# Optimization experiments

Hardware: AMD Instinct MI355X
Metric: run time of the kernel (lower is better)

## Reference

```python
import jax, jax.numpy as jnp
import numpy as np

NUM_SEGMENTS = 4480  # BATCH_SIZE * MAX_ATOMS = 64 * 70
ATOM_DIM = 64
BOND_DIM = 16
N_EDGES = 65536


def setup_inputs() -> dict:
    key = jax.random.key(0)
    k1, k2, k3, k4 = jax.random.split(key, 4)
    atom_feat = jax.random.normal(k1, (NUM_SEGMENTS, ATOM_DIM), dtype=jnp.float32)
    bond_feat = jax.random.normal(k2, (N_EDGES, BOND_DIM), dtype=jnp.float32)
    pair_idx = jax.random.randint(k3, (N_EDGES, 2), 0, NUM_SEGMENTS, dtype=jnp.int64)
    # glorot-uniform style kernel, zero bias (as in add_weight initializers)
    limit = float(np.sqrt(6.0 / (BOND_DIM + ATOM_DIM ** 2)))
    kernel = jax.random.uniform(k4, (BOND_DIM, ATOM_DIM ** 2), dtype=jnp.float32,
                                minval=-limit, maxval=limit)
    bias = jnp.zeros((ATOM_DIM ** 2,), dtype=jnp.float32)
    return {"atom_feat": atom_feat, "bond_feat": bond_feat,
            "pair_idx": pair_idx, "kernel": kernel, "bias": bias}


def reference(atom_feat, bond_feat, pair_idx, kernel, bias):
    atom_dim = atom_feat.shape[-1]
    # dense projection of bond features -> per-edge transform matrices
    bond_transformed = bond_feat @ kernel + bias               # [E, D*D]
    bond_transformed = bond_transformed.reshape(-1, atom_dim, atom_dim)  # [E, D, D]
    # gather neighbor (source) atom features per edge
    neighbor_feat = jnp.take(atom_feat, pair_idx[:, 1].astype(jnp.int32), axis=0)  # [E, D]
    # per-edge matrix-vector product
    messages = jnp.einsum('eij,ej->ei', bond_transformed, neighbor_feat)  # [E, D]
    # scatter-add into destination atoms
    return jax.ops.segment_sum(messages, pair_idx[:, 0].astype(jnp.int32),
                               num_segments=NUM_SEGMENTS)  # [NUM_SEGMENTS, D]
```

## Files before the change

kernel.cpp:

```cpp
#include <hip/hip_runtime.h>

#define NSEG   4480
#define ADIM   64
#define BDIM   16
#define NEDGE  65536
#define DPB    16
#define NBLK   (NSEG / DPB)
#define TPB    512
#define CAP    64
#define GSP    1096

#define CNT_OFF  (4u << 20)

typedef __bf16 bf16x8 __attribute__((ext_vector_type(8)));
typedef float  f32x4  __attribute__((ext_vector_type(4)));

__device__ __forceinline__ unsigned short f2bf(float f) {
    union { float f; unsigned int i; } c; c.f = f;
    unsigned int x = c.i;
    x += 0x7fffu + ((x >> 16) & 1u);
    return (unsigned short)(x >> 16);
}

union U8 { unsigned short u[8]; bf16x8 v; };

__device__ __forceinline__ bf16x8 pack_bf8(float4 a, float4 b) {
    U8 r;
    r.u[0] = f2bf(a.x); r.u[1] = f2bf(a.y); r.u[2] = f2bf(a.z); r.u[3] = f2bf(a.w);
    r.u[4] = f2bf(b.x); r.u[5] = f2bf(b.y); r.u[6] = f2bf(b.z); r.u[7] = f2bf(b.w);
    return r.v;
}

__device__ __forceinline__ void load_bond16(const float* __restrict__ bond,
                                            int e, float* bb) {
    const float4* bp = (const float4*)(bond + (size_t)e * BDIM);
    const float4 c0 = bp[0], c1 = bp[1], c2 = bp[2], c3 = bp[3];
    bb[0]=c0.x;  bb[1]=c0.y;  bb[2]=c0.z;  bb[3]=c0.w;
    bb[4]=c1.x;  bb[5]=c1.y;  bb[6]=c1.z;  bb[7]=c1.w;
    bb[8]=c2.x;  bb[9]=c2.y;  bb[10]=c2.z; bb[11]=c2.w;
    bb[12]=c3.x; bb[13]=c3.y; bb[14]=c3.z; bb[15]=c3.w;
}

__global__ __launch_bounds__(256) void scatter_kernel(
    const int* __restrict__ pair, int* __restrict__ cnt, int2* __restrict__ eb)
{
    const int e  = blockIdx.x * 256 + threadIdx.x;
    const int2 p = ((const int2*)pair)[e];
    const int idx = atomicAdd(&cnt[p.x], 1);
    if (idx < CAP) eb[(size_t)p.x * CAP + idx] = make_int2(e, p.y);
}

__global__ __launch_bounds__(TPB) void fused_kernel(
    const float* __restrict__ atom,
    const float* __restrict__ bond,
    const int*   __restrict__ cnt,
    const int2*  __restrict__ eb,
    const float* __restrict__ kern,
    const float* __restrict__ bias,
    float*       __restrict__ out)
{
    __shared__ unsigned short Gs[DPB * GSP];
    __shared__ f32x4 pb[4][64];

    const int t    = threadIdx.x;
    const int lane = t & 63;
    const int w    = t >> 6;
    const int dlo  = blockIdx.x * DPB;

    {
        const int da = dlo + 2 * w;
        const int db = da + 1;
        int na = cnt[da]; na = na < CAP ? na : CAP;
        int nb = cnt[db]; nb = nb < CAP ? nb : CAP;
        const int2 mya = eb[(size_t)da * CAP + lane];
        const int2 myb = eb[(size_t)db * CAP + lane];

        float ga[17], gb[17];
#pragma unroll
        for (int r = 0; r < 17; ++r) { ga[r] = 0.f; gb[r] = 0.f; }

        const int nmax = na > nb ? na : nb;
        for (int k = 0; k < nmax; k += 2) {
            const bool va0 = k < na, va1 = k + 1 < na;
            const bool vb0 = k < nb, vb1 = k + 1 < nb;
            int ea0 = __builtin_amdgcn_readlane(mya.x, k);
            int sa0 = __builtin_amdgcn_readlane(mya.y, k);
            int ea1 = __builtin_amdgcn_readlane(mya.x, k + 1);
            int sa1 = __builtin_amdgcn_readlane(mya.y, k + 1);
            int eb0 = __builtin_amdgcn_readlane(myb.x, k);
            int sb0 = __builtin_amdgcn_readlane(myb.y, k);
            int eb1 = __builtin_amdgcn_readlane(myb.x, k + 1);
            int sb1 = __builtin_amdgcn_readlane(myb.y, k + 1);
            ea0 = va0 ? ea0 : 0;  sa0 = va0 ? sa0 : 0;
            ea1 = va1 ? ea1 : 0;  sa1 = va1 ? sa1 : 0;
            eb0 = vb0 ? eb0 : 0;  sb0 = vb0 ? sb0 : 0;
            eb1 = vb1 ? eb1 : 0;  sb1 = vb1 ? sb1 : 0;

            const float aa0 = atom[(size_t)sa0 * ADIM + lane] * (va0 ? 1.f : 0.f);
            const float aa1 = atom[(size_t)sa1 * ADIM + lane] * (va1 ? 1.f : 0.f);
            const float ab0 = atom[(size_t)sb0 * ADIM + lane] * (vb0 ? 1.f : 0.f);
            const float ab1 = atom[(size_t)sb1 * ADIM + lane] * (vb1 ? 1.f : 0.f);
            float ba0[16], ba1[16], bb0[16], bb1[16];
            load_bond16(bond, ea0, ba0);
            load_bond16(bond, ea1, ba1);
            load_bond16(bond, eb0, bb0);
            load_bond16(bond, eb1, bb1);

#pragma unroll
            for (int r = 0; r < 16; ++r) {
                ga[r] = fmaf(aa0, ba0[r], ga[r]);
                ga[r] = fmaf(aa1, ba1[r], ga[r]);
                gb[r] = fmaf(ab0, bb0[r], gb[r]);
                gb[r] = fmaf(ab1, bb1[r], gb[r]);
            }
            ga[16] += aa0 + aa1;
            gb[16] += ab0 + ab1;
        }

#pragma unroll
        for (int r = 0; r < 17; ++r) {
            Gs[(2 * w) * GSP + r * 64 + lane]     = f2bf(ga[r]);
            Gs[(2 * w + 1) * GSP + r * 64 + lane] = f2bf(gb[r]);
        }
    }
    __syncthreads();

    {
        const int kh   = w >> 2;
        const int ct   = w & 3;
        const int m    = lane & 15;
        const int quad = lane >> 4;
        const int c    = ct * 16 + m;
        const unsigned short* Ga = Gs + (size_t)m * GSP;
        const int rlo = kh ? 9 : 0;
        const int rhi = kh ? 17 : 9;

        f32x4 acc = {0.f, 0.f, 0.f, 0.f};

        const float* ks0 = ((rlo < 16) ? (kern + (size_t)rlo * 4096) : bias)
                           + (size_t)c * 64 + quad * 8;
        float4 x0 = *(const float4*)(ks0);
        float4 x1 = *(const float4*)(ks0 + 4);
        float4 y0 = *(const float4*)(ks0 + 32);
        float4 y1 = *(const float4*)(ks0 + 36);

        for (int r = rlo; r < rhi; ++r) {
            float4 nx0 = {}, nx1 = {}, ny0 = {}, ny1 = {};
            if (r + 1 < rhi) {
                const float* ns = ((r + 1 < 16) ? (kern + (size_t)(r + 1) * 4096)
                                                : bias)
                                  + (size_t)c * 64 + quad * 8;
                nx0 = *(const float4*)(ns);
                nx1 = *(const float4*)(ns + 4);
                ny0 = *(const float4*)(ns + 32);
                ny1 = *(const float4*)(ns + 36);
            }
            const bf16x8 a0 = *(const bf16x8*)(Ga + r * 64 + quad * 8);
            const bf16x8 a1 = *(const bf16x8*)(Ga + r * 64 + 32 + quad * 8);
            acc = __builtin_amdgcn_mfma_f32_16x16x32_bf16(a0, pack_bf8(x0, x1), acc, 0, 0, 0);
            acc = __builtin_amdgcn_mfma_f32_16x16x32_bf16(a1, pack_bf8(y0, y1), acc, 0, 0, 0);
            x0 = nx0; x1 = nx1; y0 = ny0; y1 = ny1;
        }

        if (kh) pb[ct][lane] = acc;
        __syncthreads();
        if (!kh) {
            const f32x4 p = pb[ct][lane];
            acc[0] += p[0]; acc[1] += p[1]; acc[2] += p[2]; acc[3] += p[3];
#pragma unroll
            for (int rr = 0; rr < 4; ++rr)
                out[(size_t)(dlo + quad * 4 + rr) * ADIM + c] = acc[rr];
        }
    }
}

extern "C" void kernel_launch(void* const* d_in, const int* in_sizes, int n_in,
                              void* d_out, int out_size, void* d_ws, size_t ws_size,
                              hipStream_t stream) {
    const float* atom = (const float*)d_in[0];
    const float* bond = (const float*)d_in[1];
    const int*   pair = (const int*)  d_in[2];
    const float* kern = (const float*)d_in[3];
    const float* bias = (const float*)d_in[4];
    float* out = (float*)d_out;

    int2* eb  = (int2*)d_ws;
    int*  cnt = (int*)((char*)d_ws + CNT_OFF);

    hipMemsetAsync(cnt, 0, NSEG * sizeof(int), stream);
    scatter_kernel<<<NEDGE / 256, 256, 0, stream>>>(pair, cnt, eb);
    fused_kernel<<<NBLK, TPB, 0, stream>>>(atom, bond, cnt, eb, kern, bias, out);
}
```

Baseline: 112.3 us.

## Cooperatively load 16 edges per wave via LDS staging and readlane broadcast of bond features

The per-destination gather phase now has each wave load 16 edges at once. Each group of 4 lanes fetches one edge's atom row and bond vector, stages the atom rows in a per-wave LDS tile, and then broadcasts the bond values with readlane. Before, every lane redundantly loaded full 16-float bond vectors per edge. The change also processes the two destinations sequentially instead of interleaved and adds an occupancy hint to launch bounds. The cost is extra LDS traffic and many readlane instructions, and the wave-local LDS reuse relies only on a waitcnt rather than a barrier.

```diff
diff --git a/kernel.cpp b/kernel.cpp
--- a/kernel.cpp
+++ b/kernel.cpp
@@ -9,6 +9,7 @@
 #define TPB    512
 #define CAP    64
 #define GSP    1096
+#define ALP    68
 
 #define CNT_OFF  (4u << 20)
 
@@ -31,14 +32,9 @@
     return r.v;
 }
 
-__device__ __forceinline__ void load_bond16(const float* __restrict__ bond,
-                                            int e, float* bb) {
-    const float4* bp = (const float4*)(bond + (size_t)e * BDIM);
-    const float4 c0 = bp[0], c1 = bp[1], c2 = bp[2], c3 = bp[3];
-    bb[0]=c0.x;  bb[1]=c0.y;  bb[2]=c0.z;  bb[3]=c0.w;
-    bb[4]=c1.x;  bb[5]=c1.y;  bb[6]=c1.z;  bb[7]=c1.w;
-    bb[8]=c2.x;  bb[9]=c2.y;  bb[10]=c2.z; bb[11]=c2.w;
-    bb[12]=c3.x; bb[13]=c3.y; bb[14]=c3.z; bb[15]=c3.w;
+__device__ __forceinline__ float rl(float v, int l) {
+    return __builtin_bit_cast(float,
+        __builtin_amdgcn_readlane(__builtin_bit_cast(int, v), l));
 }
 
 __global__ __launch_bounds__(256) void scatter_kernel(
@@ -50,7 +46,7 @@
     if (idx < CAP) eb[(size_t)p.x * CAP + idx] = make_int2(e, p.y);
 }
 
-__global__ __launch_bounds__(TPB) void fused_kernel(
+__global__ __launch_bounds__(TPB, 4) void fused_kernel(
     const float* __restrict__ atom,
     const float* __restrict__ bond,
     const int*   __restrict__ cnt,
@@ -60,68 +56,70 @@
     float*       __restrict__ out)
 {
     __shared__ unsigned short Gs[DPB * GSP];
+    __shared__ float Al[8][16 * ALP];
     __shared__ f32x4 pb[4][64];
 
     const int t    = threadIdx.x;
     const int lane = t & 63;
     const int w    = t >> 6;
     const int dlo  = blockIdx.x * DPB;
-
-    {
-        const int da = dlo + 2 * w;
-        const int db = da + 1;
-        int na = cnt[da]; na = na < CAP ? na : CAP;
-        int nb = cnt[db]; nb = nb < CAP ? nb : CAP;
-        const int2 mya = eb[(size_t)da * CAP + lane];
-        const int2 myb = eb[(size_t)db * CAP + lane];
-
-        float ga[17], gb[17];
-#pragma unroll
-        for (int r = 0; r < 17; ++r) { ga[r] = 0.f; gb[r] = 0.f; }
-
-        const int nmax = na > nb ? na : nb;
-        for (int k = 0; k < nmax; k += 2) {
-            const bool va0 = k < na, va1 = k + 1 < na;
-            const bool vb0 = k < nb, vb1 = k + 1 < nb;
-            int ea0 = __builtin_amdgcn_readlane(mya.x, k);
-            int sa0 = __builtin_amdgcn_readlane(mya.y, k);
-            int ea1 = __builtin_amdgcn_readlane(mya.x, k + 1);
-            int sa1 = __builtin_amdgcn_readlane(mya.y, k + 1);
-            int eb0 = __builtin_amdgcn_readlane(myb.x, k);
-            int sb0 = __builtin_amdgcn_readlane(myb.y, k);
-            int eb1 = __builtin_amdgcn_readlane(myb.x, k + 1);
-            int sb1 = __builtin_amdgcn_readlane(myb.y, k + 1);
-            ea0 = va0 ? ea0 : 0;  sa0 = va0 ? sa0 : 0;
-            ea1 = va1 ? ea1 : 0;  sa1 = va1 ? sa1 : 0;
-            eb0 = vb0 ? eb0 : 0;  sb0 = vb0 ? sb0 : 0;
-            eb1 = vb1 ? eb1 : 0;  sb1 = vb1 ? sb1 : 0;
-
-            const float aa0 = atom[(size_t)sa0 * ADIM + lane] * (va0 ? 1.f : 0.f);
-            const float aa1 = atom[(size_t)sa1 * ADIM + lane] * (va1 ? 1.f : 0.f);
-            const float ab0 = atom[(size_t)sb0 * ADIM + lane] * (vb0 ? 1.f : 0.f);
-            const float ab1 = atom[(size_t)sb1 * ADIM + lane] * (vb1 ? 1.f : 0.f);
-            float ba0[16], ba1[16], bb0[16], bb1[16];
-            load_bond16(bond, ea0, ba0);
-            load_bond16(bond, ea1, ba1);
-            load_bond16(bond, eb0, bb0);
-            load_bond16(bond, eb1, bb1);
+    const int q    = lane >> 2;
+    const int p    = lane & 3;
+    float* myAl = Al[w];
 
 #pragma unroll
-            for (int r = 0; r < 16; ++r) {
-                ga[r] = fmaf(aa0, ba0[r], ga[r]);
-                ga[r] = fmaf(aa1, ba1[r], ga[r]);
-                gb[r] = fmaf(ab0, bb0[r], gb[r]);
-                gb[r] = fmaf(ab1, bb1[r], gb[r]);
+    for (int half = 0; half < 2; ++half) {
+        const int dl = 2 * w + half;
+        const int d  = dlo + dl;
+        int n = cnt[d]; n = n < CAP ? n : CAP;
+
+        float g[17];
+#pragma unroll
+        for (int r = 0; r < 17; ++r) g[r] = 0.f;
+
+        for (int kb = 0; kb < n; kb += 16) {
+            const int  slot = kb + q;
+            const bool val  = slot < n;
+            const int2 es   = eb[(size_t)d * CAP + (val ? slot : 0)];
+            const float vs  = val ? 1.f : 0.f;
+
+            const float* ap = atom + (size_t)es.y * ADIM + p * 16;
+            float4 a0 = ((const float4*)ap)[0];
+            float4 a1 = ((const float4*)ap)[1];
+            float4 a2 = ((const float4*)ap)[2];
+            float4 a3 = ((const float4*)ap)[3];
+            const float4 bq = ((const float4*)(bond + (size_t)es.x * BDIM))[p];
+
+            a0.x *= vs; a0.y *= vs; a0.z *= vs; a0.w *= vs;
+            a1.x *= vs; a1.y *= vs; a1.z *= vs; a1.w *= vs;
+            a2.x *= vs; a2.y *= vs; a2.z *= vs; a2.w *= vs;
+            a3.x *= vs; a3.y *= vs; a3.z *= vs; a3.w *= vs;
+
+            float* dst = myAl + q * ALP + p * 16;
+            ((float4*)dst)[0] = a0;
+            ((float4*)dst)[1] = a1;
+            ((float4*)dst)[2] = a2;
+            ((float4*)dst)[3] = a3;
+            __asm__ __volatile__("s_waitcnt lgkmcnt(0)" ::: "memory");
+
+#pragma unroll
+            for (int qq = 0; qq < 16; ++qq) {
+                const float a = myAl[qq * ALP + lane];
+                g[16] += a;
+#pragma unroll
+                for (int pp = 0; pp < 4; ++pp) {
+                    const int sl = 4 * qq + pp;
+                    g[pp * 4 + 0] = fmaf(rl(bq.x, sl), a, g[pp * 4 + 0]);
+                    g[pp * 4 + 1] = fmaf(rl(bq.y, sl), a, g[pp * 4 + 1]);
+                    g[pp * 4 + 2] = fmaf(rl(bq.z, sl), a, g[pp * 4 + 2]);
+                    g[pp * 4 + 3] = fmaf(rl(bq.w, sl), a, g[pp * 4 + 3]);
+                }
             }
-            ga[16] += aa0 + aa1;
-            gb[16] += ab0 + ab1;
         }
 
 #pragma unroll
-        for (int r = 0; r < 17; ++r) {
-            Gs[(2 * w) * GSP + r * 64 + lane]     = f2bf(ga[r]);
-            Gs[(2 * w + 1) * GSP + r * 64 + lane] = f2bf(gb[r]);
-        }
+        for (int r = 0; r < 17; ++r)
+            Gs[dl * GSP + r * 64 + lane] = f2bf(g[r]);
     }
     __syncthreads();
 
@@ -165,8 +163,8 @@
         if (kh) pb[ct][lane] = acc;
         __syncthreads();
         if (!kh) {
-            const f32x4 p = pb[ct][lane];
-            acc[0] += p[0]; acc[1] += p[1]; acc[2] += p[2]; acc[3] += p[3];
+            const f32x4 pr = pb[ct][lane];
+            acc[0] += pr[0]; acc[1] += pr[1]; acc[2] += pr[2]; acc[3] += pr[3];
 #pragma unroll
             for (int rr = 0; rr < 4; ++rr)
                 out[(size_t)(dlo + quad * 4 + rr) * ADIM + c] = acc[rr];
```

Result: faster. 97.73 us (-13.0%).
